# Kernel optimization log

Hardware: AMD Instinct MI355X
Metric: run time of the kernel (lower is better)

The kernel has to match this reference:

```python
import jax, jax.numpy as jnp
import numpy as np

N, M, K, D = 65536, 131072, 8, 64
TAU = 0.3
EPS = 1e-6

def setup_inputs() -> dict:
    key = jax.random.key(0)
    ks = jax.random.split(key, 16)
    s = 0.05
    return {
        "f_pts": jax.random.normal(ks[0], (N, D), jnp.float32),
        "pts": jax.random.uniform(ks[1], (N, 3), jnp.float32) * 10.0,
        "z_latent": jax.random.normal(ks[2], (M, D), jnp.float32) * 0.1,
        "centers": jax.random.uniform(ks[3], (M, 3), jnp.float32) * 10.0,
        "cand_idx": jax.random.randint(ks[4], (N, K), 0, M),
        "sim_w1": jax.random.normal(ks[5], (2 * D + 3, 64), jnp.float32) * s,
        "sim_b1": jnp.zeros((64,), jnp.float32),
        "sim_w2": jax.random.normal(ks[6], (64, 1), jnp.float32) * s,
        "sim_b2": jnp.zeros((1,), jnp.float32),
        "gate_w1": jax.random.normal(ks[7], (2 * D, D), jnp.float32) * s,
        "gate_b1": jnp.zeros((D,), jnp.float32),
        "gate_w2": jax.random.normal(ks[8], (D, 1), jnp.float32) * s,
        "gate_b2": jnp.zeros((1,), jnp.float32),
        "W_ih": jax.random.normal(ks[9], (3 * D, D), jnp.float32) * s,
        "W_hh": jax.random.normal(ks[10], (3 * D, D), jnp.float32) * s,
        "b_ih": jnp.zeros((3 * D,), jnp.float32),
        "b_hh": jnp.zeros((3 * D,), jnp.float32),
    }

def _forward(f_pts, pts, z_latent, centers, sim_w1, sim_b1, sim_w2, sim_b2,
             gate_w1, gate_b1, gate_w2, gate_b2, W_ih, W_hh, b_ih, b_hh, cand_idx):
    n, k = cand_idx.shape
    m, d = z_latent.shape
    # --- gather voxel latents / centers for each (point, candidate) pair ---
    z_c = z_latent[cand_idx]                         # (N,K,D)
    delta = pts[:, None, :] - centers[cand_idx]      # (N,K,3)
    f_b = jnp.broadcast_to(f_pts[:, None, :], (n, k, d))
    # --- similarity MLP ---
    x = jnp.concatenate([f_b, z_c, delta], axis=-1)  # (N,K,2D+3)
    h = jax.nn.relu(x @ sim_w1 + sim_b1)
    sim = (h @ sim_w2 + sim_b2)[..., 0]              # (N,K)
    # --- low-temperature top-K routing weights over candidates ---
    w = jax.nn.softmax(sim / TAU, axis=-1)           # (N,K)
    # --- scatter weighted point features to voxels ---
    flat_idx = cand_idx.reshape(-1)                  # (N*K,)
    contrib = (w[..., None] * f_pts[:, None, :]).reshape(-1, d)
    msg = jax.ops.segment_sum(contrib, flat_idx, num_segments=m)     # (M,D)
    wsum = jax.ops.segment_sum(w.reshape(-1), flat_idx, num_segments=m)
    msg = msg / (wsum[:, None] + EPS)                # normalized voxel message
    # --- per-voxel gate ---
    g_in = jnp.concatenate([z_latent, msg], axis=-1)
    gate = jax.nn.sigmoid(jax.nn.relu(g_in @ gate_w1 + gate_b1) @ gate_w2 + gate_b2)  # (M,1)
    # --- GRUCell (torch layout: rows ordered r,z,n) ---
    gi = msg @ W_ih.T + b_ih
    gh = z_latent @ W_hh.T + b_hh
    i_r, i_z, i_n = jnp.split(gi, 3, axis=-1)
    h_r, h_z, h_n = jnp.split(gh, 3, axis=-1)
    r = jax.nn.sigmoid(i_r + h_r)
    zg = jax.nn.sigmoid(i_z + h_z)
    nn_ = jnp.tanh(i_n + r * h_n)
    h_new = (1.0 - zg) * nn_ + zg * z_latent
    # gated latent update
    return z_latent + gate * (h_new - z_latent)

def reference(f_pts, pts, z_latent, centers, cand_idx, sim_w1, sim_b1, sim_w2, sim_b2,
              gate_w1, gate_b1, gate_w2, gate_b2, W_ih, W_hh, b_ih, b_hh):
    return _forward(f_pts, pts, z_latent, centers, sim_w1, sim_b1, sim_w2, sim_b2,
                    gate_w1, gate_b1, gate_w2, gate_b2, W_ih, W_hh, b_ih, b_hh, cand_idx)
```

## Files before the change

kernel.cpp:

```cpp
#include <hip/hip_runtime.h>
#include <hip/hip_fp16.h>
#include <math.h>


typedef short bf16x8 __attribute__((ext_vector_type(8)));
typedef unsigned short u16x8 __attribute__((ext_vector_type(8)));
typedef float f32x4 __attribute__((ext_vector_type(4)));
#define MFMA __builtin_amdgcn_mfma_f32_16x16x32_bf16
#define CAP 32

__device__ __forceinline__ float lane_bcast(float v, int i) {
  return __int_as_float(__builtin_amdgcn_readlane(__float_as_int(v), i));
}

__device__ __forceinline__ short f2bf(float f) {
  unsigned u = __float_as_uint(f);
  unsigned r = (u + 0x7FFFu + ((u >> 16) & 1u)) >> 16;
  return (short)r;
}

__device__ __forceinline__ float bf2f(unsigned short h) {
  return __uint_as_float(((unsigned)h) << 16);
}

__device__ __forceinline__ float sigm(float x) { return 1.0f / (1.0f + __expf(-x)); }

__global__ __launch_bounds__(256) void convert_kernel(
    const float* __restrict__ z, const float* __restrict__ f,
    unsigned short* __restrict__ zbf, unsigned short* __restrict__ fbf,
    int* __restrict__ cursor, const float* __restrict__ sim_w1,
    short* __restrict__ bfZ, short* __restrict__ bfF, long nz, long nf, int M)
{
  long tid = (long)blockIdx.x * 256 + threadIdx.x;
  long nthr = (long)gridDim.x * 256;

  for (long i = tid; i < M; i += nthr) cursor[i] = 0;

  for (long i = tid * 8; i < nz; i += nthr * 8) {
    float4 a = *(const float4*)&z[i];
    float4 b = *(const float4*)&z[i + 4];
    u16x8 o;
    o[0] = (unsigned short)f2bf(a.x); o[1] = (unsigned short)f2bf(a.y);
    o[2] = (unsigned short)f2bf(a.z); o[3] = (unsigned short)f2bf(a.w);
    o[4] = (unsigned short)f2bf(b.x); o[5] = (unsigned short)f2bf(b.y);
    o[6] = (unsigned short)f2bf(b.z); o[7] = (unsigned short)f2bf(b.w);
    *(u16x8*)&zbf[i] = o;
  }
  for (long i = tid * 8; i < nf; i += nthr * 8) {
    float4 a = *(const float4*)&f[i];
    float4 b = *(const float4*)&f[i + 4];
    u16x8 o;
    o[0] = (unsigned short)f2bf(a.x); o[1] = (unsigned short)f2bf(a.y);
    o[2] = (unsigned short)f2bf(a.z); o[3] = (unsigned short)f2bf(a.w);
    o[4] = (unsigned short)f2bf(b.x); o[5] = (unsigned short)f2bf(b.y);
    o[6] = (unsigned short)f2bf(b.z); o[7] = (unsigned short)f2bf(b.w);
    *(u16x8*)&fbf[i] = o;
  }

  if (blockIdx.x == 0 && threadIdx.x < 64) {
    int lane = threadIdx.x;
    int lr = lane & 15, lg = lane >> 4;
#pragma unroll
    for (int ct = 0; ct < 4; ++ct)
#pragma unroll
      for (int kt = 0; kt < 3; ++kt) {
        bf16x8 b;
#pragma unroll
        for (int e = 0; e < 8; ++e) {
          int k = kt * 32 + lg * 8 + e;
          float v = (k < 67) ? sim_w1[(64 + k) * 64 + ct * 16 + lr] : 0.0f;
          b[e] = f2bf(v);
        }
        *(bf16x8*)&bfZ[(ct * 3 + kt) * 512 + lane * 8] = b;
      }
#pragma unroll
    for (int ct = 0; ct < 4; ++ct)
#pragma unroll
      for (int kt = 0; kt < 2; ++kt) {
        bf16x8 b;
#pragma unroll
        for (int e = 0; e < 8; ++e) {
          int k = kt * 32 + lg * 8 + e;
          b[e] = f2bf(sim_w1[k * 64 + ct * 16 + lr]);
        }
        *(bf16x8*)&bfF[(ct * 2 + kt) * 512 + lane * 8] = b;
      }
  }
}

__global__ __launch_bounds__(256) void hb_kernel(
    const float* __restrict__ f_pts, const float* __restrict__ sim_b1,
    const short* __restrict__ bfF, unsigned short* __restrict__ HB, int npts)
{
  int wave = (blockIdx.x * 256 + threadIdx.x) >> 6;
  int lane = threadIdx.x & 63;
  int lr = lane & 15, lg = lane >> 4;
  int n0 = wave * 16;
  if (n0 >= npts) return;

  bf16x8 bf[8];
#pragma unroll
  for (int i = 0; i < 8; ++i) bf[i] = *(const bf16x8*)&bfF[i * 512 + lane * 8];

  bf16x8 a[2];
#pragma unroll
  for (int kt = 0; kt < 2; ++kt) {
    const float* src = &f_pts[(long)(n0 + lr) * 64 + kt * 32 + lg * 8];
    float4 v0 = *(const float4*)src;
    float4 v1 = *(const float4*)(src + 4);
    bf16x8 t;
    t[0] = f2bf(v0.x); t[1] = f2bf(v0.y); t[2] = f2bf(v0.z); t[3] = f2bf(v0.w);
    t[4] = f2bf(v1.x); t[5] = f2bf(v1.y); t[6] = f2bf(v1.z); t[7] = f2bf(v1.w);
    a[kt] = t;
  }

  f32x4 acc[4] = {{0,0,0,0},{0,0,0,0},{0,0,0,0},{0,0,0,0}};
#pragma unroll
  for (int ct = 0; ct < 4; ++ct) {
    acc[ct] = MFMA(a[0], bf[ct * 2 + 0], acc[ct], 0, 0, 0);
    acc[ct] = MFMA(a[1], bf[ct * 2 + 1], acc[ct], 0, 0, 0);
  }
#pragma unroll
  for (int ct = 0; ct < 4; ++ct) {
    float b1 = sim_b1[ct * 16 + lr];
#pragma unroll
    for (int e = 0; e < 4; ++e)
      HB[(long)(n0 + lg * 4 + e) * 64 + ct * 16 + lr] =
          (unsigned short)f2bf(acc[ct][e] + b1);
  }
}

#define TILES_PER_WAVE 4
__global__ __launch_bounds__(256) void pair_kernel(
    const float* __restrict__ pts, const unsigned short* __restrict__ zbf,
    const float* __restrict__ centers, const int* __restrict__ cand_idx,
    const float* __restrict__ sim_w2, const short* __restrict__ bfZ,
    const unsigned short* __restrict__ HB,
    int* __restrict__ cursor, unsigned* __restrict__ rec)
{
  int wave = (blockIdx.x * 256 + threadIdx.x) >> 6;
  int lane = threadIdx.x & 63;
  int lr = lane & 15, lg = lane >> 4;

  bf16x8 b[12];
#pragma unroll
  for (int i = 0; i < 12; ++i) b[i] = *(const bf16x8*)&bfZ[i * 512 + lane * 8];
  float w2c[4];
#pragma unroll
  for (int ct = 0; ct < 4; ++ct) w2c[ct] = sim_w2[ct * 16 + lr];

#pragma unroll 1
  for (int t = 0; t < TILES_PER_WAVE; ++t) {
    int P = (wave * TILES_PER_WAVE + t) * 16;
    int n0 = P >> 3;

    int c = cand_idx[P + lr];

    bf16x8 a[3];
#pragma unroll
    for (int kt = 0; kt < 2; ++kt)
      a[kt] = *(const bf16x8*)&zbf[(long)c * 64 + kt * 32 + lg * 8];
    {
      bf16x8 tt = {0, 0, 0, 0, 0, 0, 0, 0};
      if (lg == 0) {
        int n = n0 + (lr >> 3);
        tt[0] = f2bf(pts[n * 3 + 0] - centers[c * 3 + 0]);
        tt[1] = f2bf(pts[n * 3 + 1] - centers[c * 3 + 1]);
        tt[2] = f2bf(pts[n * 3 + 2] - centers[c * 3 + 2]);
      }
      a[2] = tt;
    }

    f32x4 acc[4] = {{0,0,0,0},{0,0,0,0},{0,0,0,0},{0,0,0,0}};
#pragma unroll
    for (int ct = 0; ct < 4; ++ct)
#pragma unroll
      for (int kt = 0; kt < 3; ++kt)
        acc[ct] = MFMA(a[kt], b[ct * 3 + kt], acc[ct], 0, 0, 0);

    int nrow = n0 + (lg >> 1);
    f32x4 part = {0.f, 0.f, 0.f, 0.f};
#pragma unroll
    for (int ct = 0; ct < 4; ++ct) {
      float hbv = bf2f(HB[(long)nrow * 64 + ct * 16 + lr]);
#pragma unroll
      for (int e = 0; e < 4; ++e) {
        float u = fmaxf(acc[ct][e] + hbv, 0.0f);
        part[e] = fmaf(u, w2c[ct], part[e]);
      }
    }
#pragma unroll
    for (int m = 1; m <= 8; m <<= 1)
#pragma unroll
      for (int e = 0; e < 4; ++e) part[e] += __shfl_xor(part[e], m, 64);

    float other[4];
#pragma unroll
    for (int e = 0; e < 4; ++e) other[e] = __shfl_xor(part[e], 16, 64);

    float mx = part[0];
#pragma unroll
    for (int e = 1; e < 4; ++e) mx = fmaxf(mx, part[e]);
#pragma unroll
    for (int e = 0; e < 4; ++e) mx = fmaxf(mx, other[e]);
    float ex[4], se = 0.f, so = 0.f;
#pragma unroll
    for (int e = 0; e < 4; ++e) {
      ex[e] = __expf((part[e] - mx) * (1.0f / 0.3f));
      se += ex[e];
      so += __expf((other[e] - mx) * (1.0f / 0.3f));
    }
    float inv = 1.0f / (se + so);
    float w[4];
#pragma unroll
    for (int e = 0; e < 4; ++e) w[e] = ex[e] * inv;

    int srcl = (lane >> 2) << 4;
    float t0 = __shfl(w[0], srcl, 64);
    float t1 = __shfl(w[1], srcl, 64);
    float t2 = __shfl(w[2], srcl, 64);
    float t3 = __shfl(w[3], srcl, 64);
    int esel = lane & 3;
    float wrow = esel == 0 ? t0 : esel == 1 ? t1 : esel == 2 ? t2 : t3;

    if (lane < 16) {
      int slot = atomicAdd(&cursor[c], 1);
      if (slot < CAP) {
        int n_pt = n0 + (lane >> 3);
        unsigned short wh = __half_as_ushort(__float2half(wrow));
        rec[(long)c * CAP + slot] = ((unsigned)n_pt << 16) | (unsigned)wh;
      }
    }
  }
}

__global__ __launch_bounds__(256) void gather_kernel(
    const unsigned* __restrict__ rec, const int* __restrict__ cursor,
    const unsigned short* __restrict__ fbf, unsigned short* __restrict__ msg_bf,
    int mvox)
{
  int tid = blockIdx.x * 256 + threadIdx.x;
  int row = tid >> 2, seg = tid & 3;
  if (row >= mvox) return;

  int cnt = cursor[row];
  cnt = cnt < CAP ? cnt : CAP;
  const unsigned* rp = &rec[(long)row * CAP];

  float acc[16];
#pragma unroll
  for (int j = 0; j < 16; ++j) acc[j] = 0.f;
  float ws = 0.f;

  for (int i = 0; i < cnt; ++i) {
    unsigned r = rp[i];
    float w = __half2float(__ushort_as_half((unsigned short)(r & 0xffffu)));
    int n = r >> 16;
    ws += w;
    const u16x8* fp = (const u16x8*)&fbf[(long)n * 64 + seg * 16];
    u16x8 f0 = fp[0], f1 = fp[1];
#pragma unroll
    for (int j = 0; j < 8; ++j) {
      acc[j]     = fmaf(w, bf2f(f0[j]), acc[j]);
      acc[8 + j] = fmaf(w, bf2f(f1[j]), acc[8 + j]);
    }
  }
  float inv = 1.0f / (ws + 1e-6f);
  u16x8 o0, o1;
#pragma unroll
  for (int j = 0; j < 8; ++j) {
    o0[j] = (unsigned short)f2bf(acc[j] * inv);
    o1[j] = (unsigned short)f2bf(acc[8 + j] * inv);
  }
  *(u16x8*)&msg_bf[(long)row * 64 + seg * 16] = o0;
  *(u16x8*)&msg_bf[(long)row * 64 + seg * 16 + 8] = o1;
}

#define AST 136
#define GST 136
#define WST 88

__global__ __launch_bounds__(512) void stage2(
    const float* __restrict__ z_latent,
    const float* __restrict__ gate_w1, const float* __restrict__ gate_b1,
    const float* __restrict__ gate_w2, const float* __restrict__ gate_b2,
    const float* __restrict__ W_ih, const float* __restrict__ W_hh,
    const float* __restrict__ b_ih, const float* __restrict__ b_hh,
    const unsigned short* __restrict__ msg_bf,
    float* __restrict__ out, int ntiles)
{
  __shared__ short Ab[128 * AST];
  __shared__ short G1t[64 * GST];
  __shared__ short Wih_l[192 * WST];
  __shared__ short Whh_l[192 * WST];
  __shared__ float gb1s[64], gw2s[64], bihs[192], bhhs[192];
  __shared__ float gb2s;

  int t = threadIdx.x;
  for (int s = t; s < 64 * 128; s += 512) {
    int j = s & 63, k = s >> 6;
    G1t[j * GST + k] = f2bf(gate_w1[s]);
  }
  for (int s = t; s < 192 * 64; s += 512) {
    int j = s >> 6, k = s & 63;
    Wih_l[j * WST + k] = f2bf(W_ih[s]);
    Whh_l[j * WST + k] = f2bf(W_hh[s]);
  }
  if (t < 64) { gb1s[t] = gate_b1[t]; gw2s[t] = gate_w2[t]; }
  if (t < 192) { bihs[t] = b_ih[t]; bhhs[t] = b_hh[t]; }
  if (t == 0) gb2s = gate_b2[0];
  __syncthreads();

  int wid = t >> 6, lane = t & 63;
  int lr = lane & 15, lg = lane >> 4;

  for (int tile = blockIdx.x; tile < ntiles; tile += gridDim.x) {
    int r0 = tile * 128;
    {
      int row = t >> 2, seg = t & 3;
      const float4* zp = (const float4*)&z_latent[(long)(r0 + row) * 64 + seg * 16];
      const u16x8* mp = (const u16x8*)&msg_bf[(long)(r0 + row) * 64 + seg * 16];
      short* az = &Ab[row * AST + seg * 16];
      short* am = &Ab[row * AST + 64 + seg * 16];
#pragma unroll
      for (int q = 0; q < 4; ++q) {
        float4 zv = zp[q];
        az[q * 4 + 0] = f2bf(zv.x); az[q * 4 + 1] = f2bf(zv.y);
        az[q * 4 + 2] = f2bf(zv.z); az[q * 4 + 3] = f2bf(zv.w);
      }
      *(u16x8*)&am[0] = mp[0];
      *(u16x8*)&am[8] = mp[1];
    }
    __syncthreads();

    int rowbase = r0 + wid * 16;
    bf16x8 a[4];
#pragma unroll
    for (int kt = 0; kt < 4; ++kt)
      a[kt] = *(const bf16x8*)&Ab[(wid * 16 + lr) * AST + kt * 32 + lg * 8];

    f32x4 hnew[4], zs[4];
    f32x4 usum = {0.f, 0.f, 0.f, 0.f};

#pragma unroll
    for (int ct = 0; ct < 4; ++ct) {
      f32x4 au = {0,0,0,0}, air = {0,0,0,0}, aiz = {0,0,0,0}, ain = {0,0,0,0};
      f32x4 ahr = {0,0,0,0}, ahz = {0,0,0,0}, ahn = {0,0,0,0};
#pragma unroll
      for (int kt = 0; kt < 4; ++kt)
        au = MFMA(a[kt], *(const bf16x8*)&G1t[(ct * 16 + lr) * GST + kt * 32 + lg * 8], au, 0, 0, 0);
#pragma unroll
      for (int k2 = 0; k2 < 2; ++k2) {
        bf16x8 amg = a[2 + k2];
        bf16x8 az_ = a[k2];
        int ko = k2 * 32 + lg * 8;
        air = MFMA(amg, *(const bf16x8*)&Wih_l[(      ct * 16 + lr) * WST + ko], air, 0, 0, 0);
        aiz = MFMA(amg, *(const bf16x8*)&Wih_l[( 64 + ct * 16 + lr) * WST + ko], aiz, 0, 0, 0);
        ain = MFMA(amg, *(const bf16x8*)&Wih_l[(128 + ct * 16 + lr) * WST + ko], ain, 0, 0, 0);
        ahr = MFMA(az_, *(const bf16x8*)&Whh_l[(      ct * 16 + lr) * WST + ko], ahr, 0, 0, 0);
        ahz = MFMA(az_, *(const bf16x8*)&Whh_l[( 64 + ct * 16 + lr) * WST + ko], ahz, 0, 0, 0);
        ahn = MFMA(az_, *(const bf16x8*)&Whh_l[(128 + ct * 16 + lr) * WST + ko], ahn, 0, 0, 0);
      }
      int c = ct * 16 + lr;
#pragma unroll
      for (int e = 0; e < 4; ++e) {
        float zv = z_latent[(long)(rowbase + lg * 4 + e) * 64 + c];
        zs[ct][e] = zv;
        float uu = fmaxf(au[e] + gb1s[c], 0.0f);
        usum[e] += uu * gw2s[c];
        float rr = sigm(air[e] + bihs[c] + ahr[e] + bhhs[c]);
        float zg = sigm(aiz[e] + bihs[64 + c] + ahz[e] + bhhs[64 + c]);
        float nn = tanhf(ain[e] + bihs[128 + c] + rr * (ahn[e] + bhhs[128 + c]));
        hnew[ct][e] = (1.0f - zg) * nn + zg * zv;
      }
    }

#pragma unroll
    for (int m = 1; m <= 8; m <<= 1)
#pragma unroll
      for (int e = 0; e < 4; ++e) {
        float v = usum[e];
        usum[e] = v + __shfl_xor(v, m, 64);
      }
    float gate[4];
#pragma unroll
    for (int e = 0; e < 4; ++e) gate[e] = sigm(usum[e] + gb2s);

#pragma unroll
    for (int ct = 0; ct < 4; ++ct)
#pragma unroll
      for (int e = 0; e < 4; ++e)
        out[(long)(rowbase + lg * 4 + e) * 64 + ct * 16 + lr] =
            zs[ct][e] + gate[e] * (hnew[ct][e] - zs[ct][e]);
    __syncthreads();
  }
}

extern "C" void kernel_launch(void* const* d_in, const int* in_sizes, int n_in,
                              void* d_out, int out_size, void* d_ws, size_t ws_size,
                              hipStream_t stream) {
  const float* f_pts   = (const float*)d_in[0];
  const float* pts     = (const float*)d_in[1];
  const float* z_lat   = (const float*)d_in[2];
  const float* centers = (const float*)d_in[3];
  const int*   cand    = (const int*)d_in[4];
  const float* sim_w1  = (const float*)d_in[5];
  const float* sim_b1  = (const float*)d_in[6];
  const float* sim_w2  = (const float*)d_in[7];
  const float* gate_w1 = (const float*)d_in[9];
  const float* gate_b1 = (const float*)d_in[10];
  const float* gate_w2 = (const float*)d_in[11];
  const float* gate_b2 = (const float*)d_in[12];
  const float* W_ih    = (const float*)d_in[13];
  const float* W_hh    = (const float*)d_in[14];
  const float* b_ih    = (const float*)d_in[15];
  const float* b_hh    = (const float*)d_in[16];

  int N = in_sizes[0] / 64;
  int M = in_sizes[2] / 64;

  int* cursor = (int*)d_ws;
  unsigned* rec = (unsigned*)(cursor + M);
  unsigned short* zbf = (unsigned short*)(rec + (size_t)M * CAP);
  unsigned short* msg_bf = zbf;
  unsigned short* fbf = zbf + (size_t)M * 64;
  unsigned short* HB = fbf + (size_t)N * 64;
  short* bfZ = (short*)(HB + (size_t)N * 64);
  short* bfF = bfZ + 12 * 512;

  convert_kernel<<<2048, 256, 0, stream>>>(z_lat, f_pts, zbf, fbf, cursor,
                                           sim_w1, bfZ, bfF,
                                           (long)M * 64, (long)N * 64, M);

  hb_kernel<<<N / 64, 256, 0, stream>>>(f_pts, sim_b1, bfF, HB, N);

  int nwaves = (N * 8) / (16 * TILES_PER_WAVE);
  pair_kernel<<<nwaves / 4, 256, 0, stream>>>(pts, zbf, centers, cand,
                                              sim_w2, bfZ, HB, cursor, rec);

  gather_kernel<<<(M * 4) / 256, 256, 0, stream>>>(rec, cursor, fbf, msg_bf, M);

  int ntiles = M / 128;
  stage2<<<256, 512, 0, stream>>>(z_lat, gate_w1, gate_b1, gate_w2, gate_b2,
                                  W_ih, W_hh, b_ih, b_hh, msg_bf,
                                  (float*)d_out, ntiles);
}
```

Measured before the change: 113.6 us.

## Fuse HB precompute into prep kernel and software-pipeline pair-kernel gathers

```diff
diff --git a/kernel.cpp b/kernel.cpp
--- a/kernel.cpp
+++ b/kernel.cpp
@@ -25,39 +25,31 @@
 
 __device__ __forceinline__ float sigm(float x) { return 1.0f / (1.0f + __expf(-x)); }
 
-__global__ __launch_bounds__(256) void convert_kernel(
+__global__ __launch_bounds__(256) void prep_kernel(
     const float* __restrict__ z, const float* __restrict__ f,
+    const float* __restrict__ sim_w1, const float* __restrict__ sim_b1,
     unsigned short* __restrict__ zbf, unsigned short* __restrict__ fbf,
-    int* __restrict__ cursor, const float* __restrict__ sim_w1,
-    short* __restrict__ bfZ, short* __restrict__ bfF, long nz, long nf, int M)
+    unsigned short* __restrict__ HB, int* __restrict__ cursor,
+    short* __restrict__ bfZ, int M)
 {
   long tid = (long)blockIdx.x * 256 + threadIdx.x;
   long nthr = (long)gridDim.x * 256;
 
   for (long i = tid; i < M; i += nthr) cursor[i] = 0;
 
+  long nz = (long)M * 64;
   for (long i = tid * 8; i < nz; i += nthr * 8) {
     float4 a = *(const float4*)&z[i];
-    float4 b = *(const float4*)&z[i + 4];
+    float4 b4 = *(const float4*)&z[i + 4];
     u16x8 o;
-    o[0] = (unsigned short)f2bf(a.x); o[1] = (unsigned short)f2bf(a.y);
-    o[2] = (unsigned short)f2bf(a.z); o[3] = (unsigned short)f2bf(a.w);
-    o[4] = (unsigned short)f2bf(b.x); o[5] = (unsigned short)f2bf(b.y);
-    o[6] = (unsigned short)f2bf(b.z); o[7] = (unsigned short)f2bf(b.w);
+    o[0] = (unsigned short)f2bf(a.x);  o[1] = (unsigned short)f2bf(a.y);
+    o[2] = (unsigned short)f2bf(a.z);  o[3] = (unsigned short)f2bf(a.w);
+    o[4] = (unsigned short)f2bf(b4.x); o[5] = (unsigned short)f2bf(b4.y);
+    o[6] = (unsigned short)f2bf(b4.z); o[7] = (unsigned short)f2bf(b4.w);
     *(u16x8*)&zbf[i] = o;
   }
-  for (long i = tid * 8; i < nf; i += nthr * 8) {
-    float4 a = *(const float4*)&f[i];
-    float4 b = *(const float4*)&f[i + 4];
-    u16x8 o;
-    o[0] = (unsigned short)f2bf(a.x); o[1] = (unsigned short)f2bf(a.y);
-    o[2] = (unsigned short)f2bf(a.z); o[3] = (unsigned short)f2bf(a.w);
-    o[4] = (unsigned short)f2bf(b.x); o[5] = (unsigned short)f2bf(b.y);
-    o[6] = (unsigned short)f2bf(b.z); o[7] = (unsigned short)f2bf(b.w);
-    *(u16x8*)&fbf[i] = o;
-  }
-
-  if (blockIdx.x == 0 && threadIdx.x < 64) {
+
+  if (blockIdx.x == gridDim.x - 1 && threadIdx.x < 64) {
     int lane = threadIdx.x;
     int lr = lane & 15, lg = lane >> 4;
 #pragma unroll
@@ -73,64 +65,58 @@
         }
         *(bf16x8*)&bfZ[(ct * 3 + kt) * 512 + lane * 8] = b;
       }
+  }
+
+  if (blockIdx.x < 1024) {
+    int wave = blockIdx.x * 4 + (threadIdx.x >> 6);
+    int lane = threadIdx.x & 63;
+    int lr = lane & 15, lg = lane >> 4;
+    int n0 = wave * 16;
+
+    bf16x8 bf[8];
 #pragma unroll
     for (int ct = 0; ct < 4; ++ct)
 #pragma unroll
       for (int kt = 0; kt < 2; ++kt) {
-        bf16x8 b;
-#pragma unroll
-        for (int e = 0; e < 8; ++e) {
-          int k = kt * 32 + lg * 8 + e;
-          b[e] = f2bf(sim_w1[k * 64 + ct * 16 + lr]);
-        }
-        *(bf16x8*)&bfF[(ct * 2 + kt) * 512 + lane * 8] = b;
-      }
-  }
-}
-
-__global__ __launch_bounds__(256) void hb_kernel(
-    const float* __restrict__ f_pts, const float* __restrict__ sim_b1,
-    const short* __restrict__ bfF, unsigned short* __restrict__ HB, int npts)
-{
-  int wave = (blockIdx.x * 256 + threadIdx.x) >> 6;
-  int lane = threadIdx.x & 63;
-  int lr = lane & 15, lg = lane >> 4;
-  int n0 = wave * 16;
-  if (n0 >= npts) return;
-
-  bf16x8 bf[8];
-#pragma unroll
-  for (int i = 0; i < 8; ++i) bf[i] = *(const bf16x8*)&bfF[i * 512 + lane * 8];
-
-  bf16x8 a[2];
-#pragma unroll
-  for (int kt = 0; kt < 2; ++kt) {
-    const float* src = &f_pts[(long)(n0 + lr) * 64 + kt * 32 + lg * 8];
-    float4 v0 = *(const float4*)src;
-    float4 v1 = *(const float4*)(src + 4);
-    bf16x8 t;
-    t[0] = f2bf(v0.x); t[1] = f2bf(v0.y); t[2] = f2bf(v0.z); t[3] = f2bf(v0.w);
-    t[4] = f2bf(v1.x); t[5] = f2bf(v1.y); t[6] = f2bf(v1.z); t[7] = f2bf(v1.w);
-    a[kt] = t;
-  }
-
-  f32x4 acc[4] = {{0,0,0,0},{0,0,0,0},{0,0,0,0},{0,0,0,0}};
-#pragma unroll
-  for (int ct = 0; ct < 4; ++ct) {
-    acc[ct] = MFMA(a[0], bf[ct * 2 + 0], acc[ct], 0, 0, 0);
-    acc[ct] = MFMA(a[1], bf[ct * 2 + 1], acc[ct], 0, 0, 0);
-  }
-#pragma unroll
-  for (int ct = 0; ct < 4; ++ct) {
-    float b1 = sim_b1[ct * 16 + lr];
-#pragma unroll
-    for (int e = 0; e < 4; ++e)
-      HB[(long)(n0 + lg * 4 + e) * 64 + ct * 16 + lr] =
-          (unsigned short)f2bf(acc[ct][e] + b1);
-  }
-}
-
-#define TILES_PER_WAVE 4
+        bf16x8 bb;
+#pragma unroll
+        for (int e = 0; e < 8; ++e)
+          bb[e] = f2bf(sim_w1[(kt * 32 + lg * 8 + e) * 64 + ct * 16 + lr]);
+        bf[ct * 2 + kt] = bb;
+      }
+
+    bf16x8 a[2];
+#pragma unroll
+    for (int kt = 0; kt < 2; ++kt) {
+      const float* src = &f[(long)(n0 + lr) * 64 + kt * 32 + lg * 8];
+      float4 v0 = *(const float4*)src;
+      float4 v1 = *(const float4*)(src + 4);
+      bf16x8 t;
+      t[0] = f2bf(v0.x); t[1] = f2bf(v0.y); t[2] = f2bf(v0.z); t[3] = f2bf(v0.w);
+      t[4] = f2bf(v1.x); t[5] = f2bf(v1.y); t[6] = f2bf(v1.z); t[7] = f2bf(v1.w);
+      a[kt] = t;
+    }
+    *(bf16x8*)&fbf[(long)(n0 + lr) * 64 + lg * 8] = a[0];
+    *(bf16x8*)&fbf[(long)(n0 + lr) * 64 + 32 + lg * 8] = a[1];
+
+    f32x4 acc[4] = {{0,0,0,0},{0,0,0,0},{0,0,0,0},{0,0,0,0}};
+#pragma unroll
+    for (int ct = 0; ct < 4; ++ct) {
+      acc[ct] = MFMA(a[0], bf[ct * 2 + 0], acc[ct], 0, 0, 0);
+      acc[ct] = MFMA(a[1], bf[ct * 2 + 1], acc[ct], 0, 0, 0);
+    }
+#pragma unroll
+    for (int ct = 0; ct < 4; ++ct) {
+      float b1 = sim_b1[ct * 16 + lr];
+#pragma unroll
+      for (int e = 0; e < 4; ++e)
+        HB[(long)(n0 + lg * 4 + e) * 64 + ct * 16 + lr] =
+            (unsigned short)f2bf(acc[ct][e] + b1);
+    }
+  }
+}
+
+#define TPW 4
 __global__ __launch_bounds__(256) void pair_kernel(
     const float* __restrict__ pts, const unsigned short* __restrict__ zbf,
     const float* __restrict__ centers, const int* __restrict__ cand_idx,
@@ -149,34 +135,47 @@
 #pragma unroll
   for (int ct = 0; ct < 4; ++ct) w2c[ct] = sim_w2[ct * 16 + lr];
 
-#pragma unroll 1
-  for (int t = 0; t < TILES_PER_WAVE; ++t) {
-    int P = (wave * TILES_PER_WAVE + t) * 16;
-    int n0 = P >> 3;
-
-    int c = cand_idx[P + lr];
-
-    bf16x8 a[3];
-#pragma unroll
-    for (int kt = 0; kt < 2; ++kt)
-      a[kt] = *(const bf16x8*)&zbf[(long)c * 64 + kt * 32 + lg * 8];
-    {
-      bf16x8 tt = {0, 0, 0, 0, 0, 0, 0, 0};
+  int call = cand_idx[wave * 64 + lane];
+
+  int c0 = __shfl(call, lr, 64);
+  bf16x8 a0 = *(const bf16x8*)&zbf[(long)c0 * 64 + lg * 8];
+  bf16x8 a1 = *(const bf16x8*)&zbf[(long)c0 * 64 + 32 + lg * 8];
+  float cx = 0, cy = 0, cz = 0, px = 0, py = 0, pz = 0;
+  if (lg == 0) {
+    cx = centers[c0 * 3 + 0]; cy = centers[c0 * 3 + 1]; cz = centers[c0 * 3 + 2];
+    int n = wave * TPW * 2 + (lr >> 3);
+    px = pts[n * 3 + 0]; py = pts[n * 3 + 1]; pz = pts[n * 3 + 2];
+  }
+
+#pragma unroll
+  for (int t = 0; t < TPW; ++t) {
+    int cn = c0; bf16x8 an0 = a0, an1 = a1;
+    float cxn = 0, cyn = 0, czn = 0, pxn = 0, pyn = 0, pzn = 0;
+    if (t + 1 < TPW) {
+      cn = __shfl(call, (t + 1) * 16 + lr, 64);
+      an0 = *(const bf16x8*)&zbf[(long)cn * 64 + lg * 8];
+      an1 = *(const bf16x8*)&zbf[(long)cn * 64 + 32 + lg * 8];
       if (lg == 0) {
-        int n = n0 + (lr >> 3);
-        tt[0] = f2bf(pts[n * 3 + 0] - centers[c * 3 + 0]);
-        tt[1] = f2bf(pts[n * 3 + 1] - centers[c * 3 + 1]);
-        tt[2] = f2bf(pts[n * 3 + 2] - centers[c * 3 + 2]);
-      }
-      a[2] = tt;
+        cxn = centers[cn * 3 + 0]; cyn = centers[cn * 3 + 1]; czn = centers[cn * 3 + 2];
+        int n = (wave * TPW + t + 1) * 2 + (lr >> 3);
+        pxn = pts[n * 3 + 0]; pyn = pts[n * 3 + 1]; pzn = pts[n * 3 + 2];
+      }
+    }
+
+    int n0 = (wave * TPW + t) * 2;
+
+    bf16x8 ad = {0, 0, 0, 0, 0, 0, 0, 0};
+    if (lg == 0) {
+      ad[0] = f2bf(px - cx); ad[1] = f2bf(py - cy); ad[2] = f2bf(pz - cz);
     }
 
     f32x4 acc[4] = {{0,0,0,0},{0,0,0,0},{0,0,0,0},{0,0,0,0}};
 #pragma unroll
-    for (int ct = 0; ct < 4; ++ct)
-#pragma unroll
-      for (int kt = 0; kt < 3; ++kt)
-        acc[ct] = MFMA(a[kt], b[ct * 3 + kt], acc[ct], 0, 0, 0);
+    for (int ct = 0; ct < 4; ++ct) {
+      acc[ct] = MFMA(a0, b[ct * 3 + 0], acc[ct], 0, 0, 0);
+      acc[ct] = MFMA(a1, b[ct * 3 + 1], acc[ct], 0, 0, 0);
+      acc[ct] = MFMA(ad, b[ct * 3 + 2], acc[ct], 0, 0, 0);
+    }
 
     int nrow = n0 + (lg >> 1);
     f32x4 part = {0.f, 0.f, 0.f, 0.f};
@@ -224,13 +223,16 @@
     float wrow = esel == 0 ? t0 : esel == 1 ? t1 : esel == 2 ? t2 : t3;
 
     if (lane < 16) {
-      int slot = atomicAdd(&cursor[c], 1);
+      int slot = atomicAdd(&cursor[c0], 1);
       if (slot < CAP) {
         int n_pt = n0 + (lane >> 3);
         unsigned short wh = __half_as_ushort(__float2half(wrow));
-        rec[(long)c * CAP + slot] = ((unsigned)n_pt << 16) | (unsigned)wh;
-      }
-    }
+        rec[(long)c0 * CAP + slot] = ((unsigned)n_pt << 16) | (unsigned)wh;
+      }
+    }
+
+    c0 = cn; a0 = an0; a1 = an1;
+    cx = cxn; cy = cyn; cz = czn; px = pxn; py = pyn; pz = pzn;
   }
 }
 
@@ -364,7 +366,7 @@
       int c = ct * 16 + lr;
 #pragma unroll
       for (int e = 0; e < 4; ++e) {
-        float zv = z_latent[(long)(rowbase + lg * 4 + e) * 64 + c];
+        float zv = bf2f((unsigned short)Ab[(wid * 16 + lg * 4 + e) * AST + c]);
         zs[ct][e] = zv;
         float uu = fmaxf(au[e] + gb1s[c], 0.0f);
         usum[e] += uu * gw2s[c];
@@ -426,17 +428,12 @@
   unsigned short* fbf = zbf + (size_t)M * 64;
   unsigned short* HB = fbf + (size_t)N * 64;
   short* bfZ = (short*)(HB + (size_t)N * 64);
-  short* bfF = bfZ + 12 * 512;
-
-  convert_kernel<<<2048, 256, 0, stream>>>(z_lat, f_pts, zbf, fbf, cursor,
-                                           sim_w1, bfZ, bfF,
-                                           (long)M * 64, (long)N * 64, M);
-
-  hb_kernel<<<N / 64, 256, 0, stream>>>(f_pts, sim_b1, bfF, HB, N);
-
-  int nwaves = (N * 8) / (16 * TILES_PER_WAVE);
-  pair_kernel<<<nwaves / 4, 256, 0, stream>>>(pts, zbf, centers, cand,
-                                              sim_w2, bfZ, HB, cursor, rec);
+
+  prep_kernel<<<2048, 256, 0, stream>>>(z_lat, f_pts, sim_w1, sim_b1,
+                                        zbf, fbf, HB, cursor, bfZ, M);
+
+  pair_kernel<<<2048, 256, 0, stream>>>(pts, zbf, centers, cand,
+                                        sim_w2, bfZ, HB, cursor, rec);
 
   gather_kernel<<<(M * 4) / 256, 256, 0, stream>>>(rec, cursor, fbf, msg_bf, M);
 
```

Result: no change. 112.6 us (-0.9%).
